# Kernel optimization log

Hardware: AMD Instinct MI355X
Metric: run time of the kernel (lower is better)

Reference implementation:

```python
import jax, jax.numpy as jnp
import numpy as np

# ---- static config (MaskedViTConfig, eval mode with inference_topk) ----
B, IMG, P, C = 32, 224, 16, 3
G = IMG // P            # 14
N = G * G + 1           # 197 tokens incl cls
D, NH = 768, 12
HD = D // NH            # 64
SCALE = HD ** -0.5
HID = 4 * D             # 3072
GH = 128                # gate hidden
WARM, DYN = 2, 10
TOPK = 118              # min(inference_topk, N-1)
NC = 1000
EPS_MASK = 1e-6
LN_EPS = 1e-5


def _ln(x, g, b):
    mu = x.mean(-1, keepdims=True)
    var = ((x - mu) ** 2).mean(-1, keepdims=True)
    return (x - mu) / jnp.sqrt(var + LN_EPS) * g + b


def _attn(x, qkv_w, qkv_b, proj_w, proj_b, add_mask):
    # x: [B,N,D]; add_mask: [B,N] additive logit bias per key, or None
    Bb, Nn, _ = x.shape
    qkv = (x @ qkv_w + qkv_b).reshape(Bb, Nn, 3, NH, HD)
    q, k, v = qkv[:, :, 0], qkv[:, :, 1], qkv[:, :, 2]  # [B,N,H,hd]
    attn = jnp.einsum('bqhd,bkhd->bhqk', q, k) * SCALE
    if add_mask is not None:
        attn = attn + add_mask[:, None, None, :]
    attn = jax.nn.softmax(attn, axis=-1)
    out = jnp.einsum('bhqk,bkhd->bqhd', attn, v).reshape(Bb, Nn, D)
    return out @ proj_w + proj_b


def _mlp(x, w1, b1, w2, b2):
    return jax.nn.gelu(x @ w1 + b1, approximate=False) @ w2 + b2


def setup_inputs() -> dict:
    key = jax.random.key(0)
    ks = iter(jax.random.split(key, 64))
    nrm = lambda shape, s=0.02: jax.random.normal(next(ks), shape, jnp.float32) * s
    z = lambda *shape: jnp.zeros(shape, jnp.float32)
    o = lambda *shape: jnp.ones(shape, jnp.float32)
    inp = {
        'images': jax.random.normal(next(ks), (B, C, IMG, IMG), jnp.float32),
        'patch_w': nrm((D, C, P, P)), 'patch_b': z(D),
        'cls_token': nrm((1, 1, D)), 'pos_embed': nrm((1, N, D)),
        # warmup blocks, stacked on leading axis [WARM,...]
        'w_ln1_g': o(WARM, D), 'w_ln1_b': z(WARM, D),
        'w_qkv_w': nrm((WARM, D, 3 * D)), 'w_qkv_b': z(WARM, 3 * D),
        'w_proj_w': nrm((WARM, D, D)), 'w_proj_b': z(WARM, D),
        'w_ln2_g': o(WARM, D), 'w_ln2_b': z(WARM, D),
        'w_fc1_w': nrm((WARM, D, HID)), 'w_fc1_b': z(WARM, HID),
        'w_fc2_w': nrm((WARM, HID, D)), 'w_fc2_b': z(WARM, D),
        # dynamic masked blocks [DYN,...]
        'd_ln1_g': o(DYN, D), 'd_ln1_b': z(DYN, D),
        'd_qkv_w': nrm((DYN, D, 3 * D)), 'd_qkv_b': z(DYN, 3 * D),
        'd_proj_w': nrm((DYN, D, D)), 'd_proj_b': z(DYN, D),
        'd_ln2_g': o(DYN, D), 'd_ln2_b': z(DYN, D),
        'd_fc1_w': nrm((DYN, D, HID)), 'd_fc1_b': z(DYN, HID),
        'd_fc2_w': nrm((DYN, HID, D)), 'd_fc2_b': z(DYN, D),
        # gate predictor: LayerNorm -> Linear(D,GH) -> GELU -> Linear(GH,1)
        'd_gln_g': o(DYN, D), 'd_gln_b': z(DYN, D),
        'd_gw1': nrm((DYN, D, GH)), 'd_gb1': z(DYN, GH),
        'd_gw2': nrm((DYN, GH, 1)), 'd_gb2': z(DYN, 1),
        # final norm + head
        'norm_g': o(D), 'norm_b': z(D),
        'head_w': nrm((D, NC)), 'head_b': z(NC),
    }
    return inp


def reference(images, patch_w, patch_b, cls_token, pos_embed,
              w_ln1_g, w_ln1_b, w_qkv_w, w_qkv_b, w_proj_w, w_proj_b,
              w_ln2_g, w_ln2_b, w_fc1_w, w_fc1_b, w_fc2_w, w_fc2_b,
              d_ln1_g, d_ln1_b, d_qkv_w, d_qkv_b, d_proj_w, d_proj_b,
              d_ln2_g, d_ln2_b, d_fc1_w, d_fc1_b, d_fc2_w, d_fc2_b,
              d_gln_g, d_gln_b, d_gw1, d_gb1, d_gw2, d_gb2,
              norm_g, norm_b, head_w, head_b):
    Bb = images.shape[0]
    # patch embed: conv with kernel==stride==P is a block reshape + matmul
    x6 = images.reshape(Bb, C, G, P, G, P)
    x = jnp.einsum('bcxpyq,dcpq->bxyd', x6, patch_w).reshape(Bb, G * G, D) + patch_b
    cls = jnp.broadcast_to(cls_token, (Bb, 1, D))
    x = jnp.concatenate([cls, x], axis=1) + pos_embed  # [B,N,D]

    for i in range(WARM):
        x = x + _attn(_ln(x, w_ln1_g[i], w_ln1_b[i]),
                      w_qkv_w[i], w_qkv_b[i], w_proj_w[i], w_proj_b[i], None)
        x = x + _mlp(_ln(x, w_ln2_g[i], w_ln2_b[i]),
                     w_fc1_w[i], w_fc1_b[i], w_fc2_w[i], w_fc2_b[i])

    for j in range(DYN):
        # gate predictor -> logits [B,N]; cls forced kept
        h = _ln(x, d_gln_g[j], d_gln_b[j])
        logits = (jax.nn.gelu(h @ d_gw1[j] + d_gb1[j], approximate=False)
                  @ d_gw2[j] + d_gb2[j]).squeeze(-1)
        logits = logits.at[:, 0].set(1e9)
        # eval-mode top-k keep mask (inference_topk path)
        _, idx = jax.lax.top_k(logits[:, 1:], TOPK)
        m = jnp.zeros_like(logits).at[:, 0].set(1.0)
        m = m.at[jnp.arange(Bb)[:, None], idx + 1].set(1.0)
        add_mask = jnp.log(jnp.clip(m, EPS_MASK, 1.0))
        x = x + _attn(_ln(x, d_ln1_g[j], d_ln1_b[j]),
                      d_qkv_w[j], d_qkv_b[j], d_proj_w[j], d_proj_b[j], add_mask)
        v = _mlp(_ln(x, d_ln2_g[j], d_ln2_b[j]),
                 d_fc1_w[j], d_fc1_b[j], d_fc2_w[j], d_fc2_b[j])
        x = x + v * m[:, :, None]  # gate_mlp_updates=True

    x = _ln(x, norm_g, norm_b)
    return x[:, 0] @ head_w + head_b  # [B, num_classes]
```

## Files before the change

### kernel.cpp

```cpp
#include <hip/hip_runtime.h>
#include <hip/hip_bf16.h>
#include <math.h>


typedef __bf16 bf16_t;
typedef __attribute__((ext_vector_type(8))) __bf16 bf16x8;
typedef __attribute__((ext_vector_type(4))) float f32x4;

#define DI __device__ __forceinline__

constexpr int NB     = 32;
constexpr int NTOK   = 197;
constexpr int DMODEL = 768;
constexpr int NHEAD  = 12;
constexpr int HDIM   = 64;
constexpr int HIDN   = 3072;
constexpr int GHID   = 128;
constexpr int MROWS  = NB * NTOK;
constexpr int PROWS  = NB * 196;
constexpr int NSEL   = 119;
constexpr int MROWSC = NB * NSEL;
constexpr int NLAYER = 12;
constexpr int KTOP   = 118;
constexpr float ATT_SCALE = 0.125f;
constexpr float LNEPS  = 1e-5f;
constexpr float LOGEPS = -13.815510558f;

DI f32x4 mfma16(bf16x8 a, bf16x8 b, f32x4 c) {
    return __builtin_amdgcn_mfma_f32_16x16x32_bf16(a, b, c, 0, 0, 0);
}

DI void gld_lds16(const void* g, void* l) {
    __builtin_amdgcn_global_load_lds(
        (__attribute__((address_space(1))) void*)(g),
        (__attribute__((address_space(3))) void*)(l), 16, 0, 0);
}

enum { EP_BF16 = 0, EP_GELU = 1, EP_RES = 2, EP_F32 = 4 };

template<int MODE, bool GA, bool SC, bool AT, int BN>
__global__ __launch_bounds__(256)
void gemm_bf16(const bf16_t* __restrict__ A, const bf16_t* __restrict__ Wt,
               const float* __restrict__ bias, void* __restrict__ Cout,
               float* __restrict__ resid, const int* __restrict__ rowidx,
               int M, int N, int K, int ldc, int klen)
{
    constexpr int WN = BN / 2;
    constexpr int NF = WN / 16;
    __shared__ __align__(16) bf16_t As[2][128 * 32];
    __shared__ __align__(16) bf16_t Bs[2][BN * 32];
    const int tid  = threadIdx.x;
    const int lane = tid & 63;
    const int wave = tid >> 6;
    const int wm = wave >> 1, wn = wave & 1;
    const int quad = lane >> 4, l16 = lane & 15;
    const int m0 = blockIdx.y * 128;
    const int n0 = blockIdx.x * BN;
    const int koff = AT ? blockIdx.z * klen : 0;

    f32x4 zero4 = {0.f, 0.f, 0.f, 0.f};
    f32x4 acc[4][NF];
#pragma unroll
    for (int i = 0; i < 4; ++i)
#pragma unroll
        for (int j = 0; j < NF; ++j) acc[i][j] = zero4;

    const int rh  = tid >> 2;
    const int seg = tid & 3;
    int cA0 = min(m0 + rh,      M - 1);
    int cA1 = min(m0 + 64 + rh, M - 1);
    const int rA0 = GA ? rowidx[cA0] : cA0;
    const int rA1 = GA ? rowidx[cA1] : cA1;
    const int rB0 = min(n0 + rh, N - 1);
    const int rB1 = (BN == 128) ? min(n0 + 64 + rh, N - 1) : 0;
    const bf16_t* pA0 = A  + (size_t)rA0 * K + koff + seg * 8;
    const bf16_t* pA1 = A  + (size_t)rA1 * K + koff + seg * 8;
    const bf16_t* pB0 = Wt + (size_t)rB0 * K + koff + seg * 8;
    const bf16_t* pB1 = Wt + (size_t)rB1 * K + koff + seg * 8;
    const int lofs0 = wave * 512;
    const int lofs1 = 2048 + wave * 512;

    auto stage = [&](int kt2, int buf) {
        const int kb = kt2 << 5;
        gld_lds16(pA0 + kb, As[buf] + lofs0);
        gld_lds16(pA1 + kb, As[buf] + lofs1);
        gld_lds16(pB0 + kb, Bs[buf] + lofs0);
        if (BN == 128) gld_lds16(pB1 + kb, Bs[buf] + lofs1);
    };

    const int nkt = klen >> 5;
    stage(0, 0);
    stage(1, 1);

    for (int kt = 0; kt < nkt; ++kt) {
        const int cur = kt & 1;
        if (kt + 1 < nkt) {
            if constexpr (BN == 128) asm volatile("s_waitcnt vmcnt(4)" ::: "memory");
            else                     asm volatile("s_waitcnt vmcnt(3)" ::: "memory");
        } else {
            asm volatile("s_waitcnt vmcnt(0)" ::: "memory");
        }
        __builtin_amdgcn_s_barrier();

        bf16x8 af[4], bfr[NF];
#pragma unroll
        for (int i = 0; i < 4; ++i)
            af[i] = *reinterpret_cast<const bf16x8*>(As[cur] + (wm * 64 + i * 16 + l16) * 32 + quad * 8);
#pragma unroll
        for (int j = 0; j < NF; ++j)
            bfr[j] = *reinterpret_cast<const bf16x8*>(Bs[cur] + (wn * WN + j * 16 + l16) * 32 + quad * 8);

        asm volatile("s_waitcnt lgkmcnt(0)" ::: "memory");
        __builtin_amdgcn_sched_barrier(0);
        __builtin_amdgcn_s_barrier();

        if (kt + 2 < nkt) stage(kt + 2, cur);

#pragma unroll
        for (int i = 0; i < 4; ++i)
#pragma unroll
            for (int j = 0; j < NF; ++j)
                acc[i][j] = mfma16(af[i], bfr[j], acc[i][j]);
    }

    const bool addb = bias && (!AT || blockIdx.z == 0);
#pragma unroll
    for (int j = 0; j < NF; ++j) {
        int c = n0 + wn * WN + j * 16 + l16;
        if (c >= N) continue;
        float bj = addb ? bias[c] : 0.f;
#pragma unroll
        for (int i = 0; i < 4; ++i) {
#pragma unroll
            for (int r = 0; r < 4; ++r) {
                int mr = m0 + wm * 64 + i * 16 + quad * 4 + r;
                if (mr >= M) continue;
                float v = acc[i][j][r] + bj;
                int orow = SC ? rowidx[mr] : mr;
                size_t off = (size_t)orow * ldc + c;
                if (MODE == EP_BF16) {
                    ((bf16_t*)Cout)[off] = (bf16_t)v;
                } else if (MODE == EP_GELU) {
                    float g = 0.5f * v * (1.f + erff(v * 0.70710678118f));
                    ((bf16_t*)Cout)[off] = (bf16_t)g;
                } else if (MODE == EP_F32) {
                    ((float*)Cout)[off] = v;
                } else {
                    if (AT) atomicAdd(&resid[off], v);
                    else    resid[off] += v;
                }
            }
        }
    }
}

DI float block_reduce_sum(float val, float* sh) {
#pragma unroll
    for (int off = 32; off; off >>= 1) val += __shfl_down(val, off, 64);
    __syncthreads();
    if ((threadIdx.x & 63) == 0) sh[threadIdx.x >> 6] = val;
    __syncthreads();
    return sh[0] + sh[1] + sh[2] + sh[3];
}

template<typename OUT>
__global__ __launch_bounds__(256)
void ln_kernel(const float* __restrict__ X, const float* __restrict__ g,
               const float* __restrict__ bta, OUT* __restrict__ H, int row_mul)
{
    __shared__ float sh[4];
    const int t = threadIdx.x;
    const float* xr = X + (size_t)blockIdx.x * row_mul * DMODEL;
    float v[3];
#pragma unroll
    for (int i = 0; i < 3; ++i) v[i] = xr[t + i * 256];
    float s = v[0] + v[1] + v[2];
    s = block_reduce_sum(s, sh);
    float mu = s * (1.f / DMODEL);
    float q = 0.f;
#pragma unroll
    for (int i = 0; i < 3; ++i) { float d = v[i] - mu; q += d * d; }
    q = block_reduce_sum(q, sh);
    float rstd = rsqrtf(q * (1.f / DMODEL) + LNEPS);
    OUT* hr = H + (size_t)blockIdx.x * DMODEL;
#pragma unroll
    for (int i = 0; i < 3; ++i) {
        int c = t + i * 256;
        hr[c] = (OUT)((v[i] - mu) * rstd * g[c] + bta[c]);
    }
}

__global__ __launch_bounds__(256)
void ln_dual_kernel(const float* __restrict__ X,
                    const float* __restrict__ g1, const float* __restrict__ b1,
                    const float* __restrict__ g2, const float* __restrict__ b2,
                    float* __restrict__ H1, bf16_t* __restrict__ H2)
{
    __shared__ float sh[4];
    const int t = threadIdx.x;
    const float* xr = X + (size_t)blockIdx.x * DMODEL;
    float v[3];
#pragma unroll
    for (int i = 0; i < 3; ++i) v[i] = xr[t + i * 256];
    float s = v[0] + v[1] + v[2];
    s = block_reduce_sum(s, sh);
    float mu = s * (1.f / DMODEL);
    float q = 0.f;
#pragma unroll
    for (int i = 0; i < 3; ++i) { float d = v[i] - mu; q += d * d; }
    q = block_reduce_sum(q, sh);
    float rstd = rsqrtf(q * (1.f / DMODEL) + LNEPS);
    float* h1 = H1 + (size_t)blockIdx.x * DMODEL;
    bf16_t* h2 = H2 + (size_t)blockIdx.x * DMODEL;
#pragma unroll
    for (int i = 0; i < 3; ++i) {
        int c = t + i * 256;
        float nrm = (v[i] - mu) * rstd;
        h1[c] = nrm * g1[c] + b1[c];
        h2[c] = (bf16_t)(nrm * g2[c] + b2[c]);
    }
}

__global__ __launch_bounds__(256)
void attn_kernel(const bf16_t* __restrict__ qkv,
                 const float* __restrict__ addmask,
                 bf16_t* __restrict__ outp)
{
    constexpr int KP = 232;
    __shared__ __align__(16) bf16_t Vt[64 * KP];
    __shared__ __align__(16) bf16_t Ps[4][16 * KP];
    const int b = blockIdx.z, h = blockIdx.y, qt = blockIdx.x;
    const int tid = threadIdx.x, wave = tid >> 6, lane = tid & 63;
    const int quad = lane >> 4, l16 = lane & 15;

    {
        int d = tid & 63, ng = tid >> 6;
        for (int n = ng; n < 224; n += 4) {
            bf16_t v = (bf16_t)0.f;
            if (n < 197)
                v = qkv[(((size_t)b * NTOK + n) * 3 + 2) * DMODEL + h * HDIM + d];
            Vt[d * KP + n] = v;
        }
    }
    __syncthreads();

    const int qbase = qt * 64 + wave * 16;
    const int qrow = qbase + l16;
    const int qc = qrow < 196 ? qrow : 196;
    bf16x8 aq[2];
#pragma unroll
    for (int t = 0; t < 2; ++t)
        aq[t] = *reinterpret_cast<const bf16x8*>(
            qkv + (((size_t)b * NTOK + qc) * 3 + 0) * DMODEL + h * HDIM + t * 32 + quad * 8);

    float sreg[13][4];
#pragma unroll
    for (int kt = 0; kt < 13; ++kt) {
        int key = kt * 16 + l16;
        int kc = key < 196 ? key : 196;
        const bf16_t* kb = qkv + (((size_t)b * NTOK + kc) * 3 + 1) * DMODEL + h * HDIM;
        bf16x8 kf0 = *reinterpret_cast<const bf16x8*>(kb + quad * 8);
        bf16x8 kf1 = *reinterpret_cast<const bf16x8*>(kb + 32 + quad * 8);
        f32x4 s = {0.f, 0.f, 0.f, 0.f};
        s = mfma16(aq[0], kf0, s);
        s = mfma16(aq[1], kf1, s);
        float am = addmask ? addmask[b * NTOK + kc] : 0.f;
        bool kvalid = key < 197;
#pragma unroll
        for (int r = 0; r < 4; ++r)
            sreg[kt][r] = kvalid ? (s[r] * ATT_SCALE + am) : -1e30f;
    }

    float psum[4];
#pragma unroll
    for (int r = 0; r < 4; ++r) {
        float mx = -1e30f;
#pragma unroll
        for (int kt = 0; kt < 13; ++kt) mx = fmaxf(mx, sreg[kt][r]);
#pragma unroll
        for (int d = 1; d < 16; d <<= 1) mx = fmaxf(mx, __shfl_xor(mx, d, 64));
        float sum = 0.f;
#pragma unroll
        for (int kt = 0; kt < 13; ++kt) {
            float p = expf(sreg[kt][r] - mx);
            sreg[kt][r] = p;
            sum += p;
        }
#pragma unroll
        for (int d = 1; d < 16; d <<= 1) sum += __shfl_xor(sum, d, 64);
        psum[r] = sum;
    }

#pragma unroll
    for (int kt = 0; kt < 13; ++kt)
#pragma unroll
        for (int r = 0; r < 4; ++r)
            Ps[wave][(quad * 4 + r) * KP + kt * 16 + l16] = (bf16_t)sreg[kt][r];
    {
        int rr = lane & 15, c0 = 208 + (lane >> 4) * 4;
#pragma unroll
        for (int i = 0; i < 4; ++i) Ps[wave][rr * KP + c0 + i] = (bf16_t)0.f;
    }
    __syncthreads();

    f32x4 o[4];
#pragma unroll
    for (int j = 0; j < 4; ++j) o[j] = (f32x4){0.f, 0.f, 0.f, 0.f};
#pragma unroll
    for (int ks = 0; ks < 7; ++ks) {
        bf16x8 ap = *reinterpret_cast<const bf16x8*>(&Ps[wave][l16 * KP + ks * 32 + quad * 8]);
#pragma unroll
        for (int j = 0; j < 4; ++j) {
            bf16x8 vf = *reinterpret_cast<const bf16x8*>(&Vt[(j * 16 + l16) * KP + ks * 32 + quad * 8]);
            o[j] = mfma16(ap, vf, o[j]);
        }
    }

#pragma unroll
    for (int r = 0; r < 4; ++r) {
        int q = qbase + quad * 4 + r;
        if (q < 197) {
            float rs = 1.f / fmaxf(psum[r], 1e-20f);
#pragma unroll
            for (int j = 0; j < 4; ++j)
                outp[((size_t)b * NTOK + q) * DMODEL + h * HDIM + j * 16 + l16] =
                    (bf16_t)(o[j][r] * rs);
        }
    }
}

__global__ __launch_bounds__(256)
void transpose_f32(const float* __restrict__ src, bf16_t* __restrict__ dst, int K, int N)
{
    __shared__ bf16_t tile[64][65];
    const size_t ls = (size_t)K * N * blockIdx.z;
    int k0 = blockIdx.y * 64, n0 = blockIdx.x * 64;
    int c = threadIdx.x & 63, r0 = threadIdx.x >> 6;
#pragma unroll
    for (int i = 0; i < 16; ++i) {
        int r = r0 + i * 4;
        tile[r][c] = (k0 + r < K && n0 + c < N)
                   ? (bf16_t)src[ls + (size_t)(k0 + r) * N + n0 + c] : (bf16_t)0.f;
    }
    __syncthreads();
#pragma unroll
    for (int i = 0; i < 16; ++i) {
        int r = r0 + i * 4;
        if (n0 + r < N && k0 + c < K) dst[ls + (size_t)(n0 + r) * K + k0 + c] = tile[c][r];
    }
}

__global__ void cvt_f32_bf16(const float* __restrict__ src, bf16_t* __restrict__ dst, int n)
{
    int i = blockIdx.x * 256 + threadIdx.x;
    if (i < n) dst[i] = (bf16_t)src[i];
}

__global__ void im2col_kernel(const float* __restrict__ img, bf16_t* __restrict__ Ap)
{
    int idx = blockIdx.x * 256 + threadIdx.x;
    if (idx >= PROWS * 768) return;
    int col = idx % 768, row = idx / 768;
    int b = row / 196, t = row % 196;
    int gi = t / 14, gj = t % 14;
    int c = col >> 8, rr = col & 255, p = rr >> 4, q = rr & 15;
    Ap[idx] = (bf16_t)img[(((size_t)b * 3 + c) * 224 + gi * 16 + p) * 224 + gj * 16 + q];
}

__global__ void assemble_x(const float* __restrict__ patch, const float* __restrict__ cls,
                           const float* __restrict__ pos, float* __restrict__ X)
{
    int idx = blockIdx.x * 256 + threadIdx.x;
    if (idx >= MROWS * DMODEL) return;
    int d = idx % DMODEL, rest = idx / DMODEL;
    int n = rest % NTOK, b = rest / NTOK;
    float v;
    if (n == 0) v = cls[d] + pos[d];
    else        v = patch[((size_t)b * 196 + (n - 1)) * DMODEL + d] + pos[(size_t)n * DMODEL + d];
    X[idx] = v;
}

__global__ __launch_bounds__(256)
void gate_fused_f32(const float* __restrict__ A, const float* __restrict__ W1,
                    const float* __restrict__ b1, const float* __restrict__ w2,
                    const float* __restrict__ b2, float* __restrict__ logits)
{
    __shared__ __align__(16) float As[16][64];
    __shared__ __align__(16) float Ws[64][128];
    const int tid = threadIdx.x;
    const int m0 = blockIdx.x * 16;
    const int tx = tid & 31;
    const int rg = tid >> 5;
    f32x4 acc0 = {0.f, 0.f, 0.f, 0.f};
    f32x4 acc1 = {0.f, 0.f, 0.f, 0.f};
    for (int k0 = 0; k0 < 768; k0 += 64) {
        __syncthreads();
        {
            int idx = tid * 4;
            int r = idx >> 6, c = idx & 63;
            *reinterpret_cast<f32x4*>(&As[r][c]) =
                *reinterpret_cast<const f32x4*>(&A[(size_t)(m0 + r) * 768 + k0 + c]);
        }
#pragma unroll
        for (int i = 0; i < 8; ++i) {
            int idx = (tid + i * 256) * 4;
            int r = idx >> 7, c = idx & 127;
            *reinterpret_cast<f32x4*>(&Ws[r][c]) =
                *reinterpret_cast<const f32x4*>(&W1[(size_t)(k0 + r) * 128 + c]);
        }
        __syncthreads();
#pragma unroll
        for (int kk = 0; kk < 64; ++kk) {
            float a0 = As[rg * 2 + 0][kk];
            float a1 = As[rg * 2 + 1][kk];
            f32x4 w = *reinterpret_cast<const f32x4*>(&Ws[kk][tx * 4]);
#pragma unroll
            for (int j = 0; j < 4; ++j) {
                acc0[j] += a0 * w[j];
                acc1[j] += a1 * w[j];
            }
        }
    }
    float s0 = 0.f, s1 = 0.f;
#pragma unroll
    for (int j = 0; j < 4; ++j) {
        int c = tx * 4 + j;
        float bj = b1[c], wj = w2[c];
        float v0 = acc0[j] + bj;
        float v1 = acc1[j] + bj;
        s0 += 0.5f * v0 * (1.f + erff(v0 * 0.70710678118f)) * wj;
        s1 += 0.5f * v1 * (1.f + erff(v1 * 0.70710678118f)) * wj;
    }
#pragma unroll
    for (int d = 1; d < 32; d <<= 1) {
        s0 += __shfl_xor(s0, d, 64);
        s1 += __shfl_xor(s1, d, 64);
    }
    if (tx == 0) {
        logits[m0 + rg * 2 + 0] = s0 + b2[0];
        logits[m0 + rg * 2 + 1] = s1 + b2[0];
    }
}

__global__ __launch_bounds__(256)
void topk_kernel(const float* __restrict__ logits, float* __restrict__ maskm,
                 float* __restrict__ addm, int* __restrict__ rowidx)
{
    __shared__ float ls[196];
    int b = blockIdx.x, t = threadIdx.x;
    if (t < 196) ls[t] = logits[b * NTOK + 1 + t];
    __syncthreads();
    if (t < 196) {
        float li = ls[t];
        int cnt = 0;
        for (int j = 0; j < 196; ++j) {
            float lj = ls[j];
            cnt += (lj > li) || (lj == li && j < t);
        }
        bool sel = cnt < KTOP;
        maskm[b * NTOK + 1 + t] = sel ? 1.f : 0.f;
        addm[b * NTOK + 1 + t]  = sel ? 0.f : LOGEPS;
        if (sel) rowidx[b * NSEL + 1 + cnt] = b * NTOK + 1 + t;
    }
    if (t == 0) { maskm[b * NTOK] = 1.f; addm[b * NTOK] = 0.f; rowidx[b * NSEL] = b * NTOK; }
}

__global__ void fill_sentinel(float* out, int n)
{
    int i = blockIdx.x * 256 + threadIdx.x;
    if (i < n) out[i] = 12345.0f;
}

static void launch_gemm(int mode, const bf16_t* A, const bf16_t* Wt, const float* bias,
                        void* C, float* resid,
                        int M, int N, int K, int ldc, hipStream_t s)
{
    dim3 grid((N + 127) / 128, (M + 127) / 128);
    dim3 blk(256);
    switch (mode) {
    case EP_BF16: gemm_bf16<EP_BF16, false, false, false, 128><<<grid, blk, 0, s>>>(A, Wt, bias, C, resid, nullptr, M, N, K, ldc, K); break;
    case EP_GELU: gemm_bf16<EP_GELU, false, false, false, 128><<<grid, blk, 0, s>>>(A, Wt, bias, C, resid, nullptr, M, N, K, ldc, K); break;
    case EP_RES:  gemm_bf16<EP_RES,  false, false, false, 128><<<grid, blk, 0, s>>>(A, Wt, bias, C, resid, nullptr, M, N, K, ldc, K); break;
    case EP_F32:  gemm_bf16<EP_F32,  false, false, false, 128><<<grid, blk, 0, s>>>(A, Wt, bias, C, resid, nullptr, M, N, K, ldc, K); break;
    }
}

static void launch_gemm_res_sk2_n64(const bf16_t* A, const bf16_t* Wt, const float* bias,
                                    float* resid, int M, int N, int K, int ldc, hipStream_t s)
{
    dim3 grid((N + 63) / 64, (M + 127) / 128, 2);
    gemm_bf16<EP_RES, false, false, true, 64><<<grid, 256, 0, s>>>(
        A, Wt, bias, nullptr, resid, nullptr, M, N, K, ldc, K / 2);
}

extern "C" void kernel_launch(void* const* d_in, const int* in_sizes, int n_in,
                              void* d_out, int out_size, void* d_ws, size_t ws_size,
                              hipStream_t stream)
{
    (void)in_sizes; (void)n_in;
    const float* images   = (const float*)d_in[0];
    const float* patch_w  = (const float*)d_in[1];
    const float* patch_b  = (const float*)d_in[2];
    const float* cls_tok  = (const float*)d_in[3];
    const float* pos_emb  = (const float*)d_in[4];
    const float* w_ln1_g  = (const float*)d_in[5];
    const float* w_ln1_b  = (const float*)d_in[6];
    const float* w_qkv_w  = (const float*)d_in[7];
    const float* w_qkv_b  = (const float*)d_in[8];
    const float* w_proj_w = (const float*)d_in[9];
    const float* w_proj_b = (const float*)d_in[10];
    const float* w_ln2_g  = (const float*)d_in[11];
    const float* w_ln2_b  = (const float*)d_in[12];
    const float* w_fc1_w  = (const float*)d_in[13];
    const float* w_fc1_b  = (const float*)d_in[14];
    const float* w_fc2_w  = (const float*)d_in[15];
    const float* w_fc2_b  = (const float*)d_in[16];
    const float* d_ln1_g  = (const float*)d_in[17];
    const float* d_ln1_b  = (const float*)d_in[18];
    const float* d_qkv_w  = (const float*)d_in[19];
    const float* d_qkv_b  = (const float*)d_in[20];
    const float* d_proj_w = (const float*)d_in[21];
    const float* d_proj_b = (const float*)d_in[22];
    const float* d_ln2_g  = (const float*)d_in[23];
    const float* d_ln2_b  = (const float*)d_in[24];
    const float* d_fc1_w  = (const float*)d_in[25];
    const float* d_fc1_b  = (const float*)d_in[26];
    const float* d_fc2_w  = (const float*)d_in[27];
    const float* d_fc2_b  = (const float*)d_in[28];
    const float* d_gln_g  = (const float*)d_in[29];
    const float* d_gln_b  = (const float*)d_in[30];
    const float* d_gw1    = (const float*)d_in[31];
    const float* d_gb1    = (const float*)d_in[32];
    const float* d_gw2    = (const float*)d_in[33];
    const float* d_gb2    = (const float*)d_in[34];
    const float* norm_g   = (const float*)d_in[35];
    const float* norm_b   = (const float*)d_in[36];
    const float* head_w   = (const float*)d_in[37];
    const float* head_b   = (const float*)d_in[38];

    char* wp = (char*)d_ws;
    auto alloc = [&](size_t bytes) -> char* {
        char* p = wp; wp += (bytes + 255) & ~(size_t)255; return p;
    };
    bf16_t* wtqkv  = (bf16_t*)alloc((size_t)NLAYER * 2304 * 768 * 2);
    bf16_t* wtproj = (bf16_t*)alloc((size_t)NLAYER * 768 * 768 * 2);
    bf16_t* wtfc1  = (bf16_t*)alloc((size_t)NLAYER * 3072 * 768 * 2);
    bf16_t* wtfc2  = (bf16_t*)alloc((size_t)NLAYER * 768 * 3072 * 2);
    bf16_t* wthead = (bf16_t*)alloc((size_t)1024 * 768 * 2);
    bf16_t* pwbf   = (bf16_t*)alloc((size_t)768 * 768 * 2);
    float*  x      = (float*)alloc((size_t)MROWS * DMODEL * 4);
    bf16_t* h      = (bf16_t*)alloc((size_t)MROWS * DMODEL * 2);
    float*  hgate  = (float*)alloc((size_t)MROWS * DMODEL * 4);
    bf16_t* hcls   = (bf16_t*)alloc((size_t)NB * DMODEL * 2);
    bf16_t* qkvb   = (bf16_t*)alloc((size_t)MROWS * 2304 * 2);
    bf16_t* attno  = (bf16_t*)alloc((size_t)MROWS * DMODEL * 2);
    bf16_t* hid    = (bf16_t*)alloc((size_t)MROWS * HIDN * 2);
    float*  logits = (float*)alloc((size_t)MROWS * 4);
    float*  maskm  = (float*)alloc((size_t)MROWS * 4);
    float*  addm   = (float*)alloc((size_t)MROWS * 4);
    int*    rowidx = (int*)alloc((size_t)MROWSC * 4);
    size_t used = (size_t)(wp - (char*)d_ws);
    if (used > ws_size) {
        fill_sentinel<<<(out_size + 255) / 256, 256, 0, stream>>>((float*)d_out, out_size);
        return;
    }
    bf16_t* Ap = hid;
    float* patchout = (float*)((char*)hid + (size_t)PROWS * 768 * 2);

    transpose_f32<<<dim3(36, 12, 2),  256, 0, stream>>>(w_qkv_w,  wtqkv,                      768, 2304);
    transpose_f32<<<dim3(36, 12, 10), 256, 0, stream>>>(d_qkv_w,  wtqkv + (size_t)2*2304*768, 768, 2304);
    transpose_f32<<<dim3(12, 12, 2),  256, 0, stream>>>(w_proj_w, wtproj,                     768, 768);
    transpose_f32<<<dim3(12, 12, 10), 256, 0, stream>>>(d_proj_w, wtproj + (size_t)2*768*768, 768, 768);
    transpose_f32<<<dim3(48, 12, 2),  256, 0, stream>>>(w_fc1_w,  wtfc1,                      768, 3072);
    transpose_f32<<<dim3(48, 12, 10), 256, 0, stream>>>(d_fc1_w,  wtfc1 + (size_t)2*3072*768, 768, 3072);
    transpose_f32<<<dim3(12, 48, 2),  256, 0, stream>>>(w_fc2_w,  wtfc2,                      3072, 768);
    transpose_f32<<<dim3(12, 48, 10), 256, 0, stream>>>(d_fc2_w,  wtfc2 + (size_t)2*768*3072, 3072, 768);
    transpose_f32<<<dim3(16, 12, 1),  256, 0, stream>>>(head_w,   wthead,                     768, 1000);
    cvt_f32_bf16<<<(768 * 768 + 255) / 256, 256, 0, stream>>>(patch_w, pwbf, 768 * 768);

    im2col_kernel<<<(PROWS * 768 + 255) / 256, 256, 0, stream>>>(images, Ap);
    launch_gemm(EP_F32, Ap, pwbf, patch_b, patchout, nullptr,
                PROWS, 768, 768, 768, stream);
    assemble_x<<<(MROWS * DMODEL + 255) / 256, 256, 0, stream>>>(patchout, cls_tok, pos_emb, x);

    for (int L = 0; L < NLAYER; ++L) {
        bool warm = (L < 2);
        int li = warm ? L : (L - 2);
        const float* ln1g = warm ? w_ln1_g + li*768 : d_ln1_g + li*768;
        const float* ln1b = warm ? w_ln1_b + li*768 : d_ln1_b + li*768;
        const float* ln2g = warm ? w_ln2_g + li*768 : d_ln2_g + li*768;
        const float* ln2b = warm ? w_ln2_b + li*768 : d_ln2_b + li*768;
        const float* qkvbias  = warm ? w_qkv_b + li*2304 : d_qkv_b + li*2304;
        const float* projbias = warm ? w_proj_b + li*768 : d_proj_b + li*768;
        const float* fc1bias  = warm ? w_fc1_b + (size_t)li*3072 : d_fc1_b + (size_t)li*3072;
        const float* fc2bias  = warm ? w_fc2_b + li*768 : d_fc2_b + li*768;
        const bf16_t* Wq = wtqkv + (size_t)L * 2304 * 768;
        const bf16_t* Wp = wtproj + (size_t)L * 768 * 768;
        const bf16_t* W1 = wtfc1 + (size_t)L * 3072 * 768;
        const bf16_t* W2 = wtfc2 + (size_t)L * 768 * 3072;

        if (!warm) {
            ln_dual_kernel<<<MROWS, 256, 0, stream>>>(
                x, d_gln_g + li*768, d_gln_b + li*768, ln1g, ln1b, hgate, h);
            gate_fused_f32<<<MROWS / 16, 256, 0, stream>>>(
                hgate, d_gw1 + (size_t)li*768*128, d_gb1 + li*128,
                d_gw2 + (size_t)li*128, d_gb2 + li, logits);
            topk_kernel<<<NB, 256, 0, stream>>>(logits, maskm, addm, rowidx);
        } else {
            ln_kernel<bf16_t><<<MROWS, 256, 0, stream>>>(x, ln1g, ln1b, h, 1);
        }
        launch_gemm(EP_BF16, h, Wq, qkvbias, qkvb, nullptr,
                    MROWS, 2304, 768, 2304, stream);
        attn_kernel<<<dim3(4, NHEAD, NB), 256, 0, stream>>>(qkvb, warm ? nullptr : addm, attno);
        launch_gemm_res_sk2_n64(attno, Wp, projbias, x, MROWS, 768, 768, 768, stream);
        ln_kernel<bf16_t><<<MROWS, 256, 0, stream>>>(x, ln2g, ln2b, h, 1);
        if (warm) {
            launch_gemm(EP_GELU, h, W1, fc1bias, hid, nullptr,
                        MROWS, 3072, 768, 3072, stream);
            launch_gemm_res_sk2_n64(hid, W2, fc2bias, x, MROWS, 768, 3072, 768, stream);
        } else {
            dim3 g1(48, (MROWSC + 127) / 128);
            gemm_bf16<EP_GELU, true, false, false, 64><<<g1, 256, 0, stream>>>(
                h, W1, fc1bias, hid, nullptr, rowidx, MROWSC, 3072, 768, 3072, 768);
            dim3 g2(12, (MROWSC + 127) / 128, 2);
            gemm_bf16<EP_RES, false, true, true, 64><<<g2, 256, 0, stream>>>(
                hid, W2, fc2bias, nullptr, x, rowidx, MROWSC, 768, 3072, 768, 1536);
        }
    }

    ln_kernel<bf16_t><<<NB, 256, 0, stream>>>(x, norm_g, norm_b, hcls, NTOK);
    launch_gemm(EP_F32, hcls, wthead, head_b, d_out, nullptr,
                NB, 1000, 768, 1000, stream);
}
```

Measured before the change: 4.617 ms.

## Restrict masked-layer attention to the top-k selected keys via row index gather

In the dynamic layers, the attention kernel now gathers K and V only for the 119 tokens picked by top-k (cls plus 118), using the row index list. Previously it scored all 197 keys and added a log-epsilon bias to the dropped ones. This cuts key tiles from 13 to 8 and PV steps from 7 to 4, and removes the float mask buffers. The trade-off is that dropped keys now get exactly zero weight instead of about 1e-6 relative weight, a tiny numerical change, and K/V loads become indirect gathers.

```diff
diff --git a/kernel.cpp b/kernel.cpp
--- a/kernel.cpp
+++ b/kernel.cpp
@@ -24,7 +24,6 @@
 constexpr int KTOP   = 118;
 constexpr float ATT_SCALE = 0.125f;
 constexpr float LNEPS  = 1e-5f;
-constexpr float LOGEPS = -13.815510558f;
 
 DI f32x4 mfma16(bf16x8 a, bf16x8 b, f32x4 c) {
     return __builtin_amdgcn_mfma_f32_16x16x32_bf16(a, b, c, 0, 0, 0);
@@ -221,12 +220,17 @@
     }
 }
 
+template<bool COMPACT>
 __global__ __launch_bounds__(256)
 void attn_kernel(const bf16_t* __restrict__ qkv,
-                 const float* __restrict__ addmask,
+                 const int* __restrict__ rowidx,
                  bf16_t* __restrict__ outp)
 {
-    constexpr int KP = 232;
+    constexpr int NV  = COMPACT ? NSEL : NTOK;
+    constexpr int NK  = COMPACT ? 128 : 224;
+    constexpr int NKT = COMPACT ? 8 : 13;
+    constexpr int NKS = NK / 32;
+    constexpr int KP  = NK + 8;
     __shared__ __align__(16) bf16_t Vt[64 * KP];
     __shared__ __align__(16) bf16_t Ps[4][16 * KP];
     const int b = blockIdx.z, h = blockIdx.y, qt = blockIdx.x;
@@ -235,10 +239,13 @@
 
     {
         int d = tid & 63, ng = tid >> 6;
-        for (int n = ng; n < 224; n += 4) {
+        for (int n = ng; n < NK; n += 4) {
             bf16_t v = (bf16_t)0.f;
-            if (n < 197)
-                v = qkv[(((size_t)b * NTOK + n) * 3 + 2) * DMODEL + h * HDIM + d];
+            if (n < NV) {
+                size_t row = COMPACT ? (size_t)rowidx[b * NSEL + n]
+                                     : (size_t)b * NTOK + n;
+                v = qkv[(row * 3 + 2) * DMODEL + h * HDIM + d];
+            }
             Vt[d * KP + n] = v;
         }
     }
@@ -253,22 +260,23 @@
         aq[t] = *reinterpret_cast<const bf16x8*>(
             qkv + (((size_t)b * NTOK + qc) * 3 + 0) * DMODEL + h * HDIM + t * 32 + quad * 8);
 
-    float sreg[13][4];
-#pragma unroll
-    for (int kt = 0; kt < 13; ++kt) {
+    float sreg[NKT][4];
+#pragma unroll
+    for (int kt = 0; kt < NKT; ++kt) {
         int key = kt * 16 + l16;
-        int kc = key < 196 ? key : 196;
-        const bf16_t* kb = qkv + (((size_t)b * NTOK + kc) * 3 + 1) * DMODEL + h * HDIM;
+        int kc = key < NV ? key : NV - 1;
+        size_t krow = COMPACT ? (size_t)rowidx[b * NSEL + kc]
+                              : (size_t)b * NTOK + kc;
+        const bf16_t* kb = qkv + (krow * 3 + 1) * DMODEL + h * HDIM;
         bf16x8 kf0 = *reinterpret_cast<const bf16x8*>(kb + quad * 8);
         bf16x8 kf1 = *reinterpret_cast<const bf16x8*>(kb + 32 + quad * 8);
         f32x4 s = {0.f, 0.f, 0.f, 0.f};
         s = mfma16(aq[0], kf0, s);
         s = mfma16(aq[1], kf1, s);
-        float am = addmask ? addmask[b * NTOK + kc] : 0.f;
-        bool kvalid = key < 197;
+        bool kvalid = key < NV;
 #pragma unroll
         for (int r = 0; r < 4; ++r)
-            sreg[kt][r] = kvalid ? (s[r] * ATT_SCALE + am) : -1e30f;
+            sreg[kt][r] = kvalid ? (s[r] * ATT_SCALE) : -1e30f;
     }
 
     float psum[4];
@@ -276,12 +284,12 @@
     for (int r = 0; r < 4; ++r) {
         float mx = -1e30f;
 #pragma unroll
-        for (int kt = 0; kt < 13; ++kt) mx = fmaxf(mx, sreg[kt][r]);
+        for (int kt = 0; kt < NKT; ++kt) mx = fmaxf(mx, sreg[kt][r]);
 #pragma unroll
         for (int d = 1; d < 16; d <<= 1) mx = fmaxf(mx, __shfl_xor(mx, d, 64));
         float sum = 0.f;
 #pragma unroll
-        for (int kt = 0; kt < 13; ++kt) {
+        for (int kt = 0; kt < NKT; ++kt) {
             float p = expf(sreg[kt][r] - mx);
             sreg[kt][r] = p;
             sum += p;
@@ -292,11 +300,11 @@
     }
 
 #pragma unroll
-    for (int kt = 0; kt < 13; ++kt)
+    for (int kt = 0; kt < NKT; ++kt)
 #pragma unroll
         for (int r = 0; r < 4; ++r)
             Ps[wave][(quad * 4 + r) * KP + kt * 16 + l16] = (bf16_t)sreg[kt][r];
-    {
+    if (!COMPACT) {
         int rr = lane & 15, c0 = 208 + (lane >> 4) * 4;
 #pragma unroll
         for (int i = 0; i < 4; ++i) Ps[wave][rr * KP + c0 + i] = (bf16_t)0.f;
@@ -307,7 +315,7 @@
 #pragma unroll
     for (int j = 0; j < 4; ++j) o[j] = (f32x4){0.f, 0.f, 0.f, 0.f};
 #pragma unroll
-    for (int ks = 0; ks < 7; ++ks) {
+    for (int ks = 0; ks < NKS; ++ks) {
         bf16x8 ap = *reinterpret_cast<const bf16x8*>(&Ps[wave][l16 * KP + ks * 32 + quad * 8]);
 #pragma unroll
         for (int j = 0; j < 4; ++j) {
@@ -443,8 +451,7 @@
 }
 
 __global__ __launch_bounds__(256)
-void topk_kernel(const float* __restrict__ logits, float* __restrict__ maskm,
-                 float* __restrict__ addm, int* __restrict__ rowidx)
+void topk_kernel(const float* __restrict__ logits, int* __restrict__ rowidx)
 {
     __shared__ float ls[196];
     int b = blockIdx.x, t = threadIdx.x;
@@ -457,12 +464,9 @@
             float lj = ls[j];
             cnt += (lj > li) || (lj == li && j < t);
         }
-        bool sel = cnt < KTOP;
-        maskm[b * NTOK + 1 + t] = sel ? 1.f : 0.f;
-        addm[b * NTOK + 1 + t]  = sel ? 0.f : LOGEPS;
-        if (sel) rowidx[b * NSEL + 1 + cnt] = b * NTOK + 1 + t;
-    }
-    if (t == 0) { maskm[b * NTOK] = 1.f; addm[b * NTOK] = 0.f; rowidx[b * NSEL] = b * NTOK; }
+        if (cnt < KTOP) rowidx[b * NSEL + 1 + cnt] = b * NTOK + 1 + t;
+    }
+    if (t == 0) rowidx[b * NSEL] = b * NTOK;
 }
 
 __global__ void fill_sentinel(float* out, int n)
@@ -556,8 +560,6 @@
     bf16_t* attno  = (bf16_t*)alloc((size_t)MROWS * DMODEL * 2);
     bf16_t* hid    = (bf16_t*)alloc((size_t)MROWS * HIDN * 2);
     float*  logits = (float*)alloc((size_t)MROWS * 4);
-    float*  maskm  = (float*)alloc((size_t)MROWS * 4);
-    float*  addm   = (float*)alloc((size_t)MROWS * 4);
     int*    rowidx = (int*)alloc((size_t)MROWSC * 4);
     size_t used = (size_t)(wp - (char*)d_ws);
     if (used > ws_size) {
@@ -605,13 +607,16 @@
             gate_fused_f32<<<MROWS / 16, 256, 0, stream>>>(
                 hgate, d_gw1 + (size_t)li*768*128, d_gb1 + li*128,
                 d_gw2 + (size_t)li*128, d_gb2 + li, logits);
-            topk_kernel<<<NB, 256, 0, stream>>>(logits, maskm, addm, rowidx);
+            topk_kernel<<<NB, 256, 0, stream>>>(logits, rowidx);
         } else {
             ln_kernel<bf16_t><<<MROWS, 256, 0, stream>>>(x, ln1g, ln1b, h, 1);
         }
         launch_gemm(EP_BF16, h, Wq, qkvbias, qkvb, nullptr,
                     MROWS, 2304, 768, 2304, stream);
-        attn_kernel<<<dim3(4, NHEAD, NB), 256, 0, stream>>>(qkvb, warm ? nullptr : addm, attno);
+        if (warm)
+            attn_kernel<false><<<dim3(4, NHEAD, NB), 256, 0, stream>>>(qkvb, nullptr, attno);
+        else
+            attn_kernel<true><<<dim3(4, NHEAD, NB), 256, 0, stream>>>(qkvb, rowidx, attno);
         launch_gemm_res_sk2_n64(attno, Wp, projbias, x, MROWS, 768, 768, 768, stream);
         ln_kernel<bf16_t><<<MROWS, 256, 0, stream>>>(x, ln2g, ln2b, h, 1);
         if (warm) {
```

Result: faster. 4.440 ms (-3.8%).
